# Performance work log

Hardware: AMD Instinct MI355X
Metric: run time of the kernel (lower is better)

The kernel has to match this reference:

```python
import jax, jax.numpy as jnp
import numpy as np

B, T, E, H, LBL = 32, 2048, 256, 256, 20


def _lstm_cell_step(x, W_ih, b_ih, b_hh):
    # Single LSTM cell step from zero state (h0=c0=0): W_hh @ h0 == 0.
    # x: [B, T, E]; W_ih: [4H, E]; gate order in torch: i, f, g, o
    gates = jnp.einsum('bte,ge->btg', x, W_ih) + b_ih + b_hh  # [B, T, 4H]
    i, f, g, o = jnp.split(gates, 4, axis=-1)
    c = jax.nn.sigmoid(i) * jnp.tanh(g)  # f * c0 == 0
    return jax.nn.sigmoid(o) * jnp.tanh(c)  # [B, T, H]


def setup_inputs() -> dict:
    key = jax.random.key(0)
    ks = jax.random.split(key, 12)
    s_ih = 1.0 / np.sqrt(H)
    inp = {
        'X': jax.random.normal(ks[0], (B, T, E), dtype=jnp.float32),
        'lengths': jax.random.randint(ks[1], (B,), 1, T + 1, dtype=jnp.int32),
        'W_ih_f': jax.random.uniform(ks[2], (4 * H, E), jnp.float32, -s_ih, s_ih),
        'b_ih_f': jax.random.uniform(ks[3], (4 * H,), jnp.float32, -s_ih, s_ih),
        'b_hh_f': jax.random.uniform(ks[4], (4 * H,), jnp.float32, -s_ih, s_ih),
        'W_ih_r': jax.random.uniform(ks[5], (4 * H, E), jnp.float32, -s_ih, s_ih),
        'b_ih_r': jax.random.uniform(ks[6], (4 * H,), jnp.float32, -s_ih, s_ih),
        'b_hh_r': jax.random.uniform(ks[7], (4 * H,), jnp.float32, -s_ih, s_ih),
        'W1': jax.random.uniform(ks[8], (256, 4 * H), jnp.float32, -1 / np.sqrt(4 * H), 1 / np.sqrt(4 * H)),
        'b1': jax.random.uniform(ks[9], (256,), jnp.float32, -1 / np.sqrt(4 * H), 1 / np.sqrt(4 * H)),
        'W2': jax.random.uniform(ks[10], (LBL, 256), jnp.float32, -1 / 16.0, 1 / 16.0),
        'b2': jax.random.uniform(ks[11], (LBL,), jnp.float32, -1 / 16.0, 1 / 16.0),
    }
    return inp


def reference(X, lengths, W_ih_f, b_ih_f, b_hh_f, W_ih_r, b_ih_r, b_hh_r, W1, b1, W2, b2):
    lengths = jnp.clip(lengths, 1, T).astype(jnp.int32)
    # Both directions are independent single-step cells (seq_len==1 in original)
    h_f = _lstm_cell_step(X, W_ih_f, b_ih_f, b_hh_f)  # [B, T, H]
    h_r = _lstm_cell_step(X, W_ih_r, b_ih_r, b_hh_r)  # [B, T, H]
    s = jnp.concatenate([h_f, h_r], axis=-1)          # [B, T, 2H]
    mask = (jnp.arange(T)[None, :] < lengths[:, None])  # [B, T]
    m = mask[:, :, None].astype(s.dtype)
    avg_pool = (s * m).sum(axis=1) / lengths[:, None].astype(s.dtype)  # [B, 2H]
    NEG = jnp.asarray(-1e30, s.dtype)
    max_pool = jnp.where(mask[:, :, None], s, NEG).max(axis=1)          # [B, 2H]
    doc = jnp.concatenate([avg_pool, max_pool], axis=-1)                # [B, 4H]
    rel = jax.nn.relu(doc)
    d1 = rel @ W1.T + b1        # dropout is identity in eval mode
    return d1 @ W2.T + b2        # [B, LBL]
```

## Files before the change

### kernel.cpp

```cpp
#include <hip/hip_runtime.h>
#include <stdint.h>

#define B_   32
#define T_   2048
#define E_   256
#define H_   256
#define LBL_ 20
#define M_   (B_ * T_)
#define NPACK_ 1536

typedef __attribute__((ext_vector_type(8))) short bf16x8;
typedef __attribute__((ext_vector_type(4))) float f32x4;

__device__ __forceinline__ unsigned short f2bf(float f) {
    union { float f; unsigned int u; } a; a.f = f;
    unsigned int u = a.u;
    u += 0x7FFFu + ((u >> 16) & 1u);
    return (unsigned short)(u >> 16);
}

__device__ __forceinline__ float rcp_(float x) {
#if __has_builtin(__builtin_amdgcn_rcpf)
    return __builtin_amdgcn_rcpf(x);
#else
    return 1.0f / x;
#endif
}
__device__ __forceinline__ float exp2_(float x) {
#if __has_builtin(__builtin_amdgcn_exp2f)
    return __builtin_amdgcn_exp2f(x);
#else
    return exp2f(x);
#endif
}
__device__ __forceinline__ float sigm_(float x) {
    return rcp_(1.f + exp2_(x * -1.44269504f));
}
__device__ __forceinline__ float tanhs_(float x) {
    return __builtin_fmaf(-2.f, rcp_(1.f + exp2_(x * 2.88539008f)), 1.f);
}
__device__ __forceinline__ float tanhp_(float c) {
    float t = c * c;
    float num = c * __builtin_fmaf(t, t + 105.f, 945.f);
    float den = __builtin_fmaf(t, __builtin_fmaf(t, 15.f, 420.f), 945.f);
    return num * rcp_(den);
}

__global__ __launch_bounds__(256) void cast_x(const float4* __restrict__ X4,
                                              uint4* __restrict__ Xb4,
                                              const int* __restrict__ lengths) {
    int b = blockIdx.y, tile = blockIdx.x;
    int lenb = lengths[b]; lenb = lenb < 1 ? 1 : (lenb > T_ ? T_ : lenb);
    int used = (lenb + 127) & ~127;
    if (tile * 8 >= used) return;
    int idx = b * 65536 + tile * 256 + threadIdx.x;
    float4 v0 = X4[2 * idx], v1 = X4[2 * idx + 1];
    union { unsigned short us[8]; uint4 u; } r;
    r.us[0] = f2bf(v0.x); r.us[1] = f2bf(v0.y); r.us[2] = f2bf(v0.z); r.us[3] = f2bf(v0.w);
    r.us[4] = f2bf(v1.x); r.us[5] = f2bf(v1.y); r.us[6] = f2bf(v1.z); r.us[7] = f2bf(v1.w);
    Xb4[idx] = r.u;
}

__global__ __launch_bounds__(256) void pack_w(
    const float* __restrict__ Wf, const float* __restrict__ bif, const float* __restrict__ bhf,
    const float* __restrict__ Wr, const float* __restrict__ bir, const float* __restrict__ bhr,
    unsigned short* __restrict__ Wp, float* __restrict__ bias_p)
{
    int n = blockIdx.x, t = threadIdx.x;
    int gidx = n / 48, r = n % 48;
    int ty = r >> 4, cc = r & 15;
    int dir = gidx >> 4, c = (gidx & 15) * 16 + cc;
    int gate = (ty == 0) ? 0 : (ty == 1 ? 2 : 3);
    int wrow = gate * 256 + c;
    const float* W = dir ? Wr : Wf;
    Wp[n * 256 + t] = f2bf(W[wrow * 256 + t]);
    if (t == 0)
        bias_p[n] = (dir ? bir[wrow] : bif[wrow]) + (dir ? bhr[wrow] : bhf[wrow]);
}

__global__ __launch_bounds__(256, 2) void gemm_pool(
    const unsigned short* __restrict__ Xb, const unsigned short* __restrict__ Wp,
    const float* __restrict__ bias_p, const int* __restrict__ lengths,
    float* __restrict__ psum, float* __restrict__ pmax)
{
    __shared__ __align__(16) short tiles[1792 * 8];
    __shared__ float red[2][4][2][16];

    short* As = tiles;
    short* Bs = tiles + 1024 * 8;

    const int tid  = threadIdx.x;
    const int w    = tid >> 6;
    const int lane = tid & 63;
    const int g    = blockIdx.x;
    const int m_tile = ((g >> 7) << 3) + (g & 7);
    const int n_tile = (g >> 3) & 15;
    const int m0   = m_tile << 7;
    const int n0   = n_tile * 96;

    const int b  = m0 >> 11;
    const int t0 = m0 & 2047;
    int lenb = lengths[b]; lenb = lenb < 1 ? 1 : (lenb > T_ ? T_ : lenb);

    if (t0 >= lenb) {
        if (tid < 32) {
            int gg = tid >> 4, c16 = tid & 15;
            int gidx = n_tile * 2 + gg;
            int col2 = (gidx >> 4) * 256 + (gidx & 15) * 16 + c16;
            int mt = m_tile & 15;
            psum[(b * 16 + mt) * 512 + col2] = 0.f;
            pmax[(b * 16 + mt) * 512 + col2] = -1e30f;
        }
        return;
    }

    const unsigned short* gp[7];
    short* lb[7];
    #pragma unroll
    for (int r = 0; r < 7; ++r) {
        int base_slot = r * 256 + w * 64;
        int s = base_slot + lane;
        int isA = (s < 1024);
        int sl = isA ? s : (s - 1024);
        int row = sl >> 3;
        int kb = (s & 7) ^ (row & 7);
        gp[r] = isA ? (Xb + (m0 + row) * 256 + kb * 8)
                    : (Wp + (n0 + row) * 256 + kb * 8);
        lb[r] = tiles + base_slot * 8;
    }

    f32x4 acc[2][6];
    #pragma unroll
    for (int i = 0; i < 2; ++i)
        #pragma unroll
        for (int j = 0; j < 6; ++j) acc[i][j] = (f32x4){0.f, 0.f, 0.f, 0.f};

    #pragma unroll
    for (int kit = 0; kit < 4; ++kit) {
        #pragma unroll
        for (int r = 0; r < 7; ++r)
            __builtin_amdgcn_global_load_lds(
                (const __attribute__((address_space(1))) void*)(gp[r] + kit * 64),
                (__attribute__((address_space(3))) void*)lb[r],
                16, 0, 0);
        __syncthreads();

        #pragma unroll
        for (int ks = 0; ks < 2; ++ks) {
            bf16x8 af[2], bfr[6];
            int kb = ks * 4 + (lane >> 4);
            #pragma unroll
            for (int rt = 0; rt < 2; ++rt) {
                int row = w * 32 + rt * 16 + (lane & 15);
                af[rt] = *(const bf16x8*)(As + (row * 8 + (kb ^ (row & 7))) * 8);
            }
            #pragma unroll
            for (int ct = 0; ct < 6; ++ct) {
                int row = ct * 16 + (lane & 15);
                bfr[ct] = *(const bf16x8*)(Bs + (row * 8 + (kb ^ (row & 7))) * 8);
            }
            #pragma unroll
            for (int rt = 0; rt < 2; ++rt)
                #pragma unroll
                for (int ct = 0; ct < 6; ++ct)
                    acc[rt][ct] = __builtin_amdgcn_mfma_f32_16x16x32_bf16(
                        af[rt], bfr[ct], acc[rt][ct], 0, 0, 0);
        }
        if (kit < 3) __syncthreads();
    }

    const int q = lane >> 4, cc = lane & 15;

    #pragma unroll
    for (int gg = 0; gg < 2; ++gg) {
        float bi = bias_p[n0 + gg * 48 + 0  + cc];
        float bg = bias_p[n0 + gg * 48 + 16 + cc];
        float bo = bias_p[n0 + gg * 48 + 32 + cc];
        float hsum = 0.f, hmax = -1e30f;
        #pragma unroll
        for (int rt = 0; rt < 2; ++rt) {
            if (t0 + w * 32 + rt * 16 >= lenb) continue;
            #pragma unroll
            for (int reg = 0; reg < 4; ++reg) {
                int row = w * 32 + rt * 16 + q * 4 + reg;
                int t = t0 + row;
                float iv = acc[rt][gg * 3 + 0][reg] + bi;
                float gv = acc[rt][gg * 3 + 1][reg] + bg;
                float ov = acc[rt][gg * 3 + 2][reg] + bo;
                float cv = sigm_(iv) * tanhs_(gv);
                float h  = sigm_(ov) * tanhp_(cv);
                if (t < lenb) { hsum += h; hmax = fmaxf(hmax, h); }
            }
        }
        hsum += __shfl_xor(hsum, 16, 64);
        hmax = fmaxf(hmax, __shfl_xor(hmax, 16, 64));
        hsum += __shfl_xor(hsum, 32, 64);
        hmax = fmaxf(hmax, __shfl_xor(hmax, 32, 64));
        if (q == 0) { red[0][w][gg][cc] = hsum; red[1][w][gg][cc] = hmax; }
    }
    __syncthreads();
    if (tid < 32) {
        int gg = tid >> 4, c16 = tid & 15;
        float s  = red[0][0][gg][c16] + red[0][1][gg][c16] + red[0][2][gg][c16] + red[0][3][gg][c16];
        float mx = fmaxf(fmaxf(red[1][0][gg][c16], red[1][1][gg][c16]),
                         fmaxf(red[1][2][gg][c16], red[1][3][gg][c16]));
        int gidx = n_tile * 2 + gg;
        int col2 = (gidx >> 4) * 256 + (gidx & 15) * 16 + c16;
        int mt = m_tile & 15;
        psum[(b * 16 + mt) * 512 + col2] = s;
        pmax[(b * 16 + mt) * 512 + col2] = mx;
    }
}

__global__ __launch_bounds__(256) void final_mlp(
    const float* __restrict__ psum, const float* __restrict__ pmax,
    const int* __restrict__ lengths,
    const float* __restrict__ W1, const float* __restrict__ b1,
    const float* __restrict__ W2, const float* __restrict__ b2,
    float* __restrict__ out)
{
    __shared__ float doc[1024];
    __shared__ float d1[256];
    int b = blockIdx.x, tid = threadIdx.x;
    int lenb = lengths[b]; lenb = lenb < 1 ? 1 : (lenb > T_ ? T_ : lenb);
    float invlen = 1.f / (float)lenb;
    for (int col = tid; col < 512; col += 256) {
        float s = 0.f, mx = -1e30f;
        #pragma unroll
        for (int mt = 0; mt < 16; ++mt) {
            s += psum[(b * 16 + mt) * 512 + col];
            mx = fmaxf(mx, pmax[(b * 16 + mt) * 512 + col]);
        }
        doc[col]       = fmaxf(s * invlen, 0.f);
        doc[512 + col] = fmaxf(mx, 0.f);
    }
    __syncthreads();
    {
        const float4* wrow = (const float4*)(W1 + tid * 1024);
        const float4* dv   = (const float4*)doc;
        float a0 = 0.f, a1 = 0.f, a2 = 0.f, a3 = 0.f;
        #pragma unroll 4
        for (int k = 0; k < 256; ++k) {
            float4 wv = wrow[k]; float4 xv = dv[k];
            a0 += wv.x * xv.x; a1 += wv.y * xv.y; a2 += wv.z * xv.z; a3 += wv.w * xv.w;
        }
        d1[tid] = a0 + a1 + a2 + a3 + b1[tid];
    }
    __syncthreads();
    if (tid < LBL_) {
        float a = b2[tid];
        const float* wr = W2 + tid * 256;
        #pragma unroll 8
        for (int k = 0; k < 256; ++k) a += wr[k] * d1[k];
        out[b * LBL_ + tid] = a;
    }
}

#define XB_OFF   0u
#define WP_OFF   33554432u
#define BIAS_OFF 34340864u
#define PSUM_OFF 34347008u
#define PMAX_OFF 35395584u

extern "C" void kernel_launch(void* const* d_in, const int* in_sizes, int n_in,
                              void* d_out, int out_size, void* d_ws, size_t ws_size,
                              hipStream_t stream) {
    (void)in_sizes; (void)n_in; (void)out_size; (void)ws_size;
    const float* X      = (const float*)d_in[0];
    const int*   lens   = (const int*)d_in[1];
    const float* W_ih_f = (const float*)d_in[2];
    const float* b_ih_f = (const float*)d_in[3];
    const float* b_hh_f = (const float*)d_in[4];
    const float* W_ih_r = (const float*)d_in[5];
    const float* b_ih_r = (const float*)d_in[6];
    const float* b_hh_r = (const float*)d_in[7];
    const float* W1     = (const float*)d_in[8];
    const float* b1     = (const float*)d_in[9];
    const float* W2     = (const float*)d_in[10];
    const float* b2     = (const float*)d_in[11];
    float* out = (float*)d_out;

    char* ws = (char*)d_ws;
    unsigned short* Xb     = (unsigned short*)(ws + XB_OFF);
    unsigned short* Wp     = (unsigned short*)(ws + WP_OFF);
    float*          bias_p = (float*)(ws + BIAS_OFF);
    float*          psum   = (float*)(ws + PSUM_OFF);
    float*          pmax   = (float*)(ws + PMAX_OFF);

    cast_x<<<dim3(256, 32), 256, 0, stream>>>((const float4*)X, (uint4*)Xb, lens);
    pack_w<<<NPACK_, 256, 0, stream>>>(W_ih_f, b_ih_f, b_hh_f, W_ih_r, b_ih_r, b_hh_r,
                                       Wp, bias_p);
    gemm_pool<<<dim3(8192), 256, 0, stream>>>(Xb, Wp, bias_p, lens, psum, pmax);
    final_mlp<<<B_, 256, 0, stream>>>(psum, pmax, lens, W1, b1, W2, b2, out);
}
```

Baseline: 201.1 us.

## Double-buffer GEMM LDS tiles, merge prep kernels, split final MLP

Merges the X cast and weight pack kernels into one launch. Double-buffers the LDS tiles in gemm_pool so the next K-slice's global-to-LDS load is issued before the current slice's MFMAs, and drops the trailing barrier. It also splits the final MLP into two kernels so more blocks share the W1 matvec. The costs are doubled LDS use, which may reduce occupancy at 2 blocks per CU, plus one extra launch for the MLP. A single barrier per iteration may also let the prefetch overwrite the buffer that was read in the previous iteration.

```diff
diff --git a/kernel.cpp b/kernel.cpp
--- a/kernel.cpp
+++ b/kernel.cpp
@@ -46,36 +46,37 @@
     return num * rcp_(den);
 }
 
-__global__ __launch_bounds__(256) void cast_x(const float4* __restrict__ X4,
-                                              uint4* __restrict__ Xb4,
-                                              const int* __restrict__ lengths) {
-    int b = blockIdx.y, tile = blockIdx.x;
-    int lenb = lengths[b]; lenb = lenb < 1 ? 1 : (lenb > T_ ? T_ : lenb);
-    int used = (lenb + 127) & ~127;
-    if (tile * 8 >= used) return;
-    int idx = b * 65536 + tile * 256 + threadIdx.x;
-    float4 v0 = X4[2 * idx], v1 = X4[2 * idx + 1];
-    union { unsigned short us[8]; uint4 u; } r;
-    r.us[0] = f2bf(v0.x); r.us[1] = f2bf(v0.y); r.us[2] = f2bf(v0.z); r.us[3] = f2bf(v0.w);
-    r.us[4] = f2bf(v1.x); r.us[5] = f2bf(v1.y); r.us[6] = f2bf(v1.z); r.us[7] = f2bf(v1.w);
-    Xb4[idx] = r.u;
-}
-
-__global__ __launch_bounds__(256) void pack_w(
+__global__ __launch_bounds__(256) void prep(
+    const float4* __restrict__ X4, uint4* __restrict__ Xb4,
+    const int* __restrict__ lengths,
     const float* __restrict__ Wf, const float* __restrict__ bif, const float* __restrict__ bhf,
     const float* __restrict__ Wr, const float* __restrict__ bir, const float* __restrict__ bhr,
     unsigned short* __restrict__ Wp, float* __restrict__ bias_p)
 {
-    int n = blockIdx.x, t = threadIdx.x;
-    int gidx = n / 48, r = n % 48;
-    int ty = r >> 4, cc = r & 15;
-    int dir = gidx >> 4, c = (gidx & 15) * 16 + cc;
-    int gate = (ty == 0) ? 0 : (ty == 1 ? 2 : 3);
-    int wrow = gate * 256 + c;
-    const float* W = dir ? Wr : Wf;
-    Wp[n * 256 + t] = f2bf(W[wrow * 256 + t]);
-    if (t == 0)
-        bias_p[n] = (dir ? bir[wrow] : bif[wrow]) + (dir ? bhr[wrow] : bhf[wrow]);
+    int bi = blockIdx.x;
+    if (bi < 8192) {
+        int b = bi >> 8, tile = bi & 255;
+        int lenb = lengths[b]; lenb = lenb < 1 ? 1 : (lenb > T_ ? T_ : lenb);
+        int used = (lenb + 127) & ~127;
+        if (tile * 8 >= used) return;
+        int idx = b * 65536 + tile * 256 + threadIdx.x;
+        float4 v0 = X4[2 * idx], v1 = X4[2 * idx + 1];
+        union { unsigned short us[8]; uint4 u; } r;
+        r.us[0] = f2bf(v0.x); r.us[1] = f2bf(v0.y); r.us[2] = f2bf(v0.z); r.us[3] = f2bf(v0.w);
+        r.us[4] = f2bf(v1.x); r.us[5] = f2bf(v1.y); r.us[6] = f2bf(v1.z); r.us[7] = f2bf(v1.w);
+        Xb4[idx] = r.u;
+    } else {
+        int n = bi - 8192, t = threadIdx.x;
+        int gidx = n / 48, r = n % 48;
+        int ty = r >> 4, cc = r & 15;
+        int dir = gidx >> 4, c = (gidx & 15) * 16 + cc;
+        int gate = (ty == 0) ? 0 : (ty == 1 ? 2 : 3);
+        int wrow = gate * 256 + c;
+        const float* W = dir ? Wr : Wf;
+        Wp[n * 256 + t] = f2bf(W[wrow * 256 + t]);
+        if (t == 0)
+            bias_p[n] = (dir ? bir[wrow] : bif[wrow]) + (dir ? bhr[wrow] : bhf[wrow]);
+    }
 }
 
 __global__ __launch_bounds__(256, 2) void gemm_pool(
@@ -83,11 +84,8 @@
     const float* __restrict__ bias_p, const int* __restrict__ lengths,
     float* __restrict__ psum, float* __restrict__ pmax)
 {
-    __shared__ __align__(16) short tiles[1792 * 8];
+    __shared__ __align__(16) short tiles[2][1792 * 8];
     __shared__ float red[2][4][2][16];
-
-    short* As = tiles;
-    short* Bs = tiles + 1024 * 8;
 
     const int tid  = threadIdx.x;
     const int w    = tid >> 6;
@@ -115,7 +113,7 @@
     }
 
     const unsigned short* gp[7];
-    short* lb[7];
+    int lbs[7];
     #pragma unroll
     for (int r = 0; r < 7; ++r) {
         int base_slot = r * 256 + w * 64;
@@ -126,7 +124,7 @@
         int kb = (s & 7) ^ (row & 7);
         gp[r] = isA ? (Xb + (m0 + row) * 256 + kb * 8)
                     : (Wp + (n0 + row) * 256 + kb * 8);
-        lb[r] = tiles + base_slot * 8;
+        lbs[r] = base_slot * 8;
     }
 
     f32x4 acc[2][6];
@@ -136,14 +134,25 @@
         for (int j = 0; j < 6; ++j) acc[i][j] = (f32x4){0.f, 0.f, 0.f, 0.f};
 
     #pragma unroll
+    for (int r = 0; r < 7; ++r)
+        __builtin_amdgcn_global_load_lds(
+            (const __attribute__((address_space(1))) void*)(gp[r]),
+            (__attribute__((address_space(3))) void*)(&tiles[0][0] + lbs[r]),
+            16, 0, 0);
+
+    #pragma unroll
     for (int kit = 0; kit < 4; ++kit) {
-        #pragma unroll
-        for (int r = 0; r < 7; ++r)
-            __builtin_amdgcn_global_load_lds(
-                (const __attribute__((address_space(1))) void*)(gp[r] + kit * 64),
-                (__attribute__((address_space(3))) void*)lb[r],
-                16, 0, 0);
         __syncthreads();
+        if (kit < 3) {
+            #pragma unroll
+            for (int r = 0; r < 7; ++r)
+                __builtin_amdgcn_global_load_lds(
+                    (const __attribute__((address_space(1))) void*)(gp[r] + (kit + 1) * 64),
+                    (__attribute__((address_space(3))) void*)(&tiles[(kit + 1) & 1][0] + lbs[r]),
+                    16, 0, 0);
+        }
+        const short* As = &tiles[kit & 1][0];
+        const short* Bs = As + 1024 * 8;
 
         #pragma unroll
         for (int ks = 0; ks < 2; ++ks) {
@@ -166,7 +175,6 @@
                     acc[rt][ct] = __builtin_amdgcn_mfma_f32_16x16x32_bf16(
                         af[rt], bfr[ct], acc[rt][ct], 0, 0, 0);
         }
-        if (kit < 3) __syncthreads();
     }
 
     const int q = lane >> 4, cc = lane & 15;
@@ -212,16 +220,14 @@
     }
 }
 
-__global__ __launch_bounds__(256) void final_mlp(
+__global__ __launch_bounds__(256) void mlp1(
     const float* __restrict__ psum, const float* __restrict__ pmax,
     const int* __restrict__ lengths,
     const float* __restrict__ W1, const float* __restrict__ b1,
-    const float* __restrict__ W2, const float* __restrict__ b2,
-    float* __restrict__ out)
+    float* __restrict__ d1g)
 {
     __shared__ float doc[1024];
-    __shared__ float d1[256];
-    int b = blockIdx.x, tid = threadIdx.x;
+    int nt = blockIdx.x, b = blockIdx.y, tid = threadIdx.x;
     int lenb = lengths[b]; lenb = lenb < 1 ? 1 : (lenb > T_ ? T_ : lenb);
     float invlen = 1.f / (float)lenb;
     for (int col = tid; col < 512; col += 256) {
@@ -235,25 +241,46 @@
         doc[512 + col] = fmaxf(mx, 0.f);
     }
     __syncthreads();
-    {
-        const float4* wrow = (const float4*)(W1 + tid * 1024);
-        const float4* dv   = (const float4*)doc;
-        float a0 = 0.f, a1 = 0.f, a2 = 0.f, a3 = 0.f;
-        #pragma unroll 4
-        for (int k = 0; k < 256; ++k) {
-            float4 wv = wrow[k]; float4 xv = dv[k];
-            a0 += wv.x * xv.x; a1 += wv.y * xv.y; a2 += wv.z * xv.z; a3 += wv.w * xv.w;
-        }
-        d1[tid] = a0 + a1 + a2 + a3 + b1[tid];
-    }
+    int neuron = tid >> 2, tq = tid & 3;
+    int row = nt * 64 + neuron;
+    const float4* wrow = (const float4*)(W1 + row * 1024 + tq * 256);
+    const float4* dv   = (const float4*)doc + tq * 64;
+    float a0 = 0.f, a1 = 0.f, a2 = 0.f, a3 = 0.f;
+    #pragma unroll 4
+    for (int k = 0; k < 64; ++k) {
+        float4 wv = wrow[k]; float4 xv = dv[k];
+        a0 += wv.x * xv.x; a1 += wv.y * xv.y; a2 += wv.z * xv.z; a3 += wv.w * xv.w;
+    }
+    float a = a0 + a1 + a2 + a3;
+    a += __shfl_xor(a, 1, 64);
+    a += __shfl_xor(a, 2, 64);
+    if (tq == 0) d1g[b * 256 + row] = a + b1[row];
+}
+
+__global__ __launch_bounds__(256) void mlp2(
+    const float* __restrict__ d1g,
+    const float* __restrict__ W2, const float* __restrict__ b2,
+    float* __restrict__ out)
+{
+    __shared__ float d1s[256];
+    int b = blockIdx.x, tid = threadIdx.x;
+    d1s[tid] = d1g[b * 256 + tid];
     __syncthreads();
-    if (tid < LBL_) {
-        float a = b2[tid];
-        const float* wr = W2 + tid * 256;
-        #pragma unroll 8
-        for (int k = 0; k < 256; ++k) a += wr[k] * d1[k];
-        out[b * LBL_ + tid] = a;
-    }
+    int j = tid >> 3, tq = tid & 7;
+    float a = 0.f;
+    if (j < LBL_) {
+        const float4* wr = (const float4*)(W2 + j * 256) + tq * 8;
+        const float4* dd = (const float4*)d1s + tq * 8;
+        #pragma unroll
+        for (int k = 0; k < 8; ++k) {
+            float4 wv = wr[k]; float4 xv = dd[k];
+            a += wv.x * xv.x + wv.y * xv.y + wv.z * xv.z + wv.w * xv.w;
+        }
+    }
+    a += __shfl_xor(a, 1, 64);
+    a += __shfl_xor(a, 2, 64);
+    a += __shfl_xor(a, 4, 64);
+    if (j < LBL_ && tq == 0) out[b * LBL_ + j] = a + b2[j];
 }
 
 #define XB_OFF   0u
@@ -261,6 +288,7 @@
 #define BIAS_OFF 34340864u
 #define PSUM_OFF 34347008u
 #define PMAX_OFF 35395584u
+#define D1_OFF   36444160u
 
 extern "C" void kernel_launch(void* const* d_in, const int* in_sizes, int n_in,
                               void* d_out, int out_size, void* d_ws, size_t ws_size,
@@ -286,10 +314,12 @@
     float*          bias_p = (float*)(ws + BIAS_OFF);
     float*          psum   = (float*)(ws + PSUM_OFF);
     float*          pmax   = (float*)(ws + PMAX_OFF);
-
-    cast_x<<<dim3(256, 32), 256, 0, stream>>>((const float4*)X, (uint4*)Xb, lens);
-    pack_w<<<NPACK_, 256, 0, stream>>>(W_ih_f, b_ih_f, b_hh_f, W_ih_r, b_ih_r, b_hh_r,
-                                       Wp, bias_p);
+    float*          d1g    = (float*)(ws + D1_OFF);
+
+    prep<<<dim3(8192 + NPACK_), 256, 0, stream>>>(
+        (const float4*)X, (uint4*)Xb, lens,
+        W_ih_f, b_ih_f, b_hh_f, W_ih_r, b_ih_r, b_hh_r, Wp, bias_p);
     gemm_pool<<<dim3(8192), 256, 0, stream>>>(Xb, Wp, bias_p, lens, psum, pmax);
-    final_mlp<<<B_, 256, 0, stream>>>(psum, pmax, lens, W1, b1, W2, b2, out);
-}
+    mlp1<<<dim3(4, 32), 256, 0, stream>>>(psum, pmax, lens, W1, b1, d1g);
+    mlp2<<<dim3(B_), 256, 0, stream>>>(d1g, W2, b2, out);
+}
```

New measurement: 198.6 us. No clear change (-1.2%).
